# Optimization experiments

Hardware: AMD Instinct MI355X
Metric: run time of the kernel (lower is better)

Reference implementation:

```python
import jax, jax.numpy as jnp
import numpy as np

D_MODEL = 2048
D_STATE = 16
D_CONV = 4
EXPAND = 2
D_INNER = EXPAND * D_MODEL  # 4096
DT_RANK = 128               # ceil(2048/16)
BATCH = 2
SEQ = 1024


def setup_inputs() -> dict:
    key = jax.random.key(0)
    ks = jax.random.split(key, 10)
    n = lambda k, shape, scale: jax.random.normal(k, shape, dtype=jnp.float32) * scale
    # A_log = log(arange(1..N)) broadcast over channels, exactly as in the torch init
    A_log = jnp.log(jnp.tile(jnp.arange(1, D_STATE + 1, dtype=jnp.float32)[None, :], (D_INNER, 1)))
    return {
        "hidden_states": n(ks[0], (BATCH, SEQ, D_MODEL), 1.0),
        "W_in": n(ks[1], (2 * D_INNER, D_MODEL), 0.02),
        "conv_w": n(ks[2], (D_INNER, D_CONV), 0.2),
        "conv_b": n(ks[3], (D_INNER,), 0.02),
        "W_x": n(ks[4], (DT_RANK + 2 * D_STATE, D_INNER), 0.02),
        "W_dt": n(ks[5], (D_INNER, DT_RANK), 0.05),
        "b_dt": n(ks[6], (D_INNER,), 0.5) - 4.0,  # softplus(b_dt) ~ small dt, like inv-softplus init
        "A_log": A_log,
        "D_skip": jnp.ones((D_INNER,), jnp.float32),
        "W_out": n(ks[7], (D_MODEL, D_INNER), 0.02),
    }


def _mamba_forward(hidden_states, W_in, conv_w, conv_b, W_x, W_dt, b_dt, A_log, D_skip, W_out):
    B, L, _ = hidden_states.shape
    # in_proj then split into x (SSM path) and z (gate)
    xz = hidden_states @ W_in.T                      # (B, L, 2*Di)
    x, z = jnp.split(xz, 2, axis=-1)                 # (B, L, Di) each
    # causal depthwise conv1d (kernel D_CONV, left pad D_CONV-1) + SiLU
    xp = jnp.pad(x, ((0, 0), (D_CONV - 1, 0), (0, 0)))
    xc = conv_b
    for k in range(D_CONV):
        xc = xc + conv_w[:, k] * xp[:, k:k + L, :]
    x = jax.nn.silu(xc)                              # (B, L, Di)
    # input-dependent dt, B, C
    x_dbl = x @ W_x.T                                # (B, L, dt_rank + 2N)
    dt_low, B_in, C_in = jnp.split(x_dbl, [DT_RANK, DT_RANK + D_STATE], axis=-1)
    dt = dt_low @ W_dt.T                             # (B, L, Di); bias added inside scan (delta_bias)
    delta = jax.nn.softplus(dt + b_dt)               # (B, L, Di)
    A = -jnp.exp(A_log)                              # (Di, N)

    def step(h, inp):
        delta_t, u_t, B_t, C_t = inp                 # (B,Di),(B,Di),(B,N),(B,N)
        dA = jnp.exp(delta_t[..., None] * A)         # (B, Di, N)
        h = dA * h + (delta_t * u_t)[..., None] * B_t[:, None, :]
        y_t = jnp.einsum('bdn,bn->bd', h, C_t)
        return h, y_t

    h0 = jnp.zeros((B, D_INNER, D_STATE), x.dtype)
    xs = (jnp.swapaxes(delta, 0, 1), jnp.swapaxes(x, 0, 1),
          jnp.swapaxes(B_in, 0, 1), jnp.swapaxes(C_in, 0, 1))
    _, ys = jax.lax.scan(step, h0, xs)               # ys: (L, B, Di)
    y = jnp.swapaxes(ys, 0, 1)                       # (B, L, Di)
    y = y + D_skip * x                               # skip connection
    y = y * jax.nn.silu(z)                           # output gating
    return y @ W_out.T                               # (B, L, D_MODEL)


def reference(hidden_states, W_in, conv_w, conv_b, W_x, W_dt, b_dt, A_log, D_skip, W_out):
    return _mamba_forward(hidden_states, W_in, conv_w, conv_b, W_x, W_dt, b_dt, A_log, D_skip, W_out)
```

## Files before the change

### kernel.cpp

```cpp
#include <hip/hip_runtime.h>
#include <hip/hip_bf16.h>


#define BATCH 2
#define SEQ 1024
#define DMODEL 2048
#define DINNER 4096
#define DSTATE 16
#define DTRANK 128
#define ROWS (BATCH * SEQ)
#define XDBL_N (DTRANK + 2 * DSTATE)
#define NCHUNK 32
#define LOG2_NCHUNK 5
#define CLEN (SEQ / NCHUNK)
#define WXPAD 192
#define SPLITK 16

typedef unsigned short ushort_t;
typedef __attribute__((ext_vector_type(8))) short short8;
typedef __attribute__((ext_vector_type(4))) float f32x4;

__device__ __forceinline__ ushort_t bf16_rne(float f) {
  unsigned u = __float_as_uint(f);
  return (ushort_t)((u + 0x7FFFu + ((u >> 16) & 1u)) >> 16);
}

__global__ __launch_bounds__(256) void cast_bf16(
    const float* __restrict__ x, ushort_t* __restrict__ o, int n4) {
  int i = blockIdx.x * 256 + threadIdx.x;
  if (i >= n4) return;
  float4 v = ((const float4*)x)[i];
  ushort4 h;
  h.x = bf16_rne(v.x); h.y = bf16_rne(v.y);
  h.z = bf16_rne(v.z); h.w = bf16_rne(v.w);
  ((ushort4*)o)[i] = h;
}

__global__ __launch_bounds__(256) void cast_wx(
    const float* __restrict__ wx, ushort_t* __restrict__ o) {
  int i = blockIdx.x * 256 + threadIdx.x;
  if (i >= WXPAD * (DINNER / 4)) return;
  int row = i >> 10;
  ushort4 h = {0, 0, 0, 0};
  if (row < XDBL_N) {
    float4 v = ((const float4*)wx)[i];
    h.x = bf16_rne(v.x); h.y = bf16_rne(v.y);
    h.z = bf16_rne(v.z); h.w = bf16_rne(v.w);
  }
  ((ushort4*)o)[i] = h;
}

template <int TM, int TN, int EPI, bool SK, bool SWZ>
__global__ __launch_bounds__(256, 2) void gemm_bf16(
    const ushort_t* __restrict__ X, int lda,
    const ushort_t* __restrict__ W, int ldb,
    const float* __restrict__ bias,
    float* __restrict__ C, int ldc, int kslice, size_t sstride) {
  constexpr int MI = TM / 32;
  constexpr int NI = TN / 32;
  constexpr int G = (TM + TN) / 32;
  __shared__ __attribute__((aligned(16))) ushort_t lds[(TM + TN) * 64];

  const int tid = threadIdx.x;
  const int lane = tid & 63;
  const int w = tid >> 6;
  const int wm = w & 1, wn = w >> 1;
  int bx = blockIdx.x, by = blockIdx.y;
  if (SWZ) {
    const int bid = by * 16 + bx;
    const int cpx = (16 * gridDim.y) >> 3;
    const int sz = (bid & 7) * cpx + (bid >> 3);
    bx = sz & 15;
    by = sz >> 4;
  }
  const int m0 = bx * TM;
  const int n0 = by * TN;
  const int kbase = SK ? blockIdx.z * kslice : 0;

  const int lrow = lane >> 3;
  const int csw = (lane & 7) ^ lrow;
  const int quad = lane >> 4;
  const int l15 = lane & 15;
  const int x0 = quad ^ (lane & 7);
  const int baseA = (wm * (TM / 2) + l15) * 64;
  const int baseB = (TM + wn * (TN / 2) + l15) * 64;

  f32x4 acc[MI][NI] = {};

  for (int kt = 0; kt < kslice; kt += 64) {
#pragma unroll
    for (int j = 0; j < G; j++) {
      const int r0 = (w * G + j) * 8;
      const int row = r0 + lrow;
      const ushort_t* src = (r0 < TM)
          ? X + (size_t)(m0 + row) * lda + kbase + kt + csw * 8
          : W + (size_t)(n0 + row - TM) * ldb + kbase + kt + csw * 8;
      __builtin_amdgcn_global_load_lds(
          (const __attribute__((address_space(1))) unsigned int*)src,
          (__attribute__((address_space(3))) unsigned int*)&lds[r0 * 64],
          16, 0, 0);
    }
    __syncthreads();

#pragma unroll
    for (int ks = 0; ks < 2; ks++) {
      const int xo = (x0 ^ (ks * 4)) * 8;
      short8 a[MI], b[NI];
#pragma unroll
      for (int mi = 0; mi < MI; mi++)
        a[mi] = *(const short8*)&lds[baseA + mi * 1024 + xo];
#pragma unroll
      for (int ni = 0; ni < NI; ni++)
        b[ni] = *(const short8*)&lds[baseB + ni * 1024 + xo];
#pragma unroll
      for (int mi = 0; mi < MI; mi++)
#pragma unroll
        for (int ni = 0; ni < NI; ni++)
          acc[mi][ni] = __builtin_amdgcn_mfma_f32_16x16x32_bf16(
              a[mi], b[ni], acc[mi][ni], 0, 0, 0);
    }
    __syncthreads();
  }

  float* Cs = SK ? (C + (size_t)blockIdx.z * sstride) : C;
#pragma unroll
  for (int mi = 0; mi < MI; mi++)
#pragma unroll
    for (int ni = 0; ni < NI; ni++) {
      int row = m0 + wm * (TM / 2) + mi * 16 + quad * 4;
      int col = n0 + wn * (TN / 2) + ni * 16 + l15;
#pragma unroll
      for (int r = 0; r < 4; r++) {
        float v = acc[mi][ni][r];
        if (EPI == 1) {
          v += bias[col];
          v = (v > 20.f) ? v : log1pf(__expf(v));
        }
        Cs[(size_t)(row + r) * ldc + col] = v;
      }
    }
}

__device__ __forceinline__ void bar() {
  asm volatile("" ::: "memory");
  __builtin_amdgcn_s_barrier();
  asm volatile("" ::: "memory");
}
#define VMWAIT(n) asm volatile("s_waitcnt vmcnt(" #n ")" ::: "memory")
#define LGKM0 asm volatile("s_waitcnt lgkmcnt(0)" ::: "memory")
#define LGKM8 asm volatile("s_waitcnt lgkmcnt(8)" ::: "memory")
#define SCHED0 __builtin_amdgcn_sched_barrier(0)

#define CLUSTER(AF, BF, MH, NH)                                           \
  do {                                                                    \
    __builtin_amdgcn_s_setprio(1);                                        \
    _Pragma("unroll")                                                     \
    for (int mi = 0; mi < 4; mi++)                                        \
      _Pragma("unroll")                                                   \
      for (int ni = 0; ni < 2; ni++)                                      \
        _Pragma("unroll")                                                 \
        for (int ks = 0; ks < 2; ks++)                                    \
          acc[(MH) * 4 + mi][(NH) * 2 + ni] =                             \
              __builtin_amdgcn_mfma_f32_16x16x32_bf16(                    \
                  AF[mi][ks], BF[ni][ks],                                 \
                  acc[(MH) * 4 + mi][(NH) * 2 + ni], 0, 0, 0);            \
    __builtin_amdgcn_s_setprio(0);                                        \
  } while (0)

#define RD_A(buf, half)                                                   \
  _Pragma("unroll")                                                       \
  for (int mi = 0; mi < 4; mi++)                                          \
    _Pragma("unroll")                                                     \
    for (int ks = 0; ks < 2; ks++) a[mi][ks] = rdA(buf, half, mi, ks)

#define RD_B(dst, buf, nh)                                                \
  _Pragma("unroll")                                                       \
  for (int ni = 0; ni < 2; ni++)                                          \
    _Pragma("unroll")                                                     \
    for (int ks = 0; ks < 2; ks++) dst[ni][ks] = rdB(buf, nh, ni, ks)

__global__ __launch_bounds__(512, 2) void gemm256(
    const ushort_t* __restrict__ X, int lda,
    const ushort_t* __restrict__ W, int ldb,
    float* __restrict__ C, int ldc, int K) {
  __shared__ __attribute__((aligned(16))) ushort_t lds[65536];
  const int tid = threadIdx.x;
  const int lane = tid & 63;
  const int w = tid >> 6;
  const int wm = w >> 2, wn = w & 3;
  const int bid = blockIdx.y * 8 + blockIdx.x;
  const int swz = (bid & 7) * 32 + (bid >> 3);
  const int m0 = (swz & 7) * 256;
  const int n0 = (swz >> 3) * 256;
  const int lrow = lane >> 3;
  const int csw = (lane & 7) ^ lrow;
  const int quad = lane >> 4;
  const int l15 = lane & 15;
  const int sx = lane & 7;

  f32x4 acc[8][4] = {};
  short8 a[4][2], b0[2][2], b1[2][2];

  const ushort_t* Asrc = X + (size_t)(m0 + w * 8 + lrow) * lda + csw * 8;
  const ushort_t* Bsrc = W + (size_t)(n0 + w * 8 + lrow) * ldb + csw * 8;

  auto stA = [&](int buf, int g, int kt) {
    __builtin_amdgcn_global_load_lds(
        (const __attribute__((address_space(1))) unsigned int*)
            (Asrc + (size_t)g * 64 * lda + kt),
        (__attribute__((address_space(3))) unsigned int*)
            &lds[buf * 16384 + (g * 64 + w * 8) * 64],
        16, 0, 0);
  };
  auto stB = [&](int buf, int g, int kt) {
    __builtin_amdgcn_global_load_lds(
        (const __attribute__((address_space(1))) unsigned int*)
            (Bsrc + (size_t)g * 64 * ldb + kt),
        (__attribute__((address_space(3))) unsigned int*)
            &lds[32768 + buf * 16384 + (g * 64 + w * 8) * 64],
        16, 0, 0);
  };
  auto rdA = [&](int buf, int half, int mi, int ks) {
    int row = wm * 128 + half * 64 + mi * 16 + l15;
    int ch = (ks * 4 + quad) ^ sx;
    return *(const short8*)&lds[buf * 16384 + row * 64 + ch * 8];
  };
  auto rdB = [&](int buf, int nh, int ni, int ks) {
    int row = nh * 128 + wn * 32 + ni * 16 + l15;
    int ch = (ks * 4 + quad) ^ sx;
    return *(const short8*)&lds[32768 + buf * 16384 + row * 64 + ch * 8];
  };

#pragma unroll
  for (int g = 0; g < 4; g++) stA(0, g, 0);
#pragma unroll
  for (int g = 0; g < 4; g++) stB(0, g, 0);
  stA(1, 0, 64); stA(1, 2, 64);
  stB(1, 0, 64); stB(1, 1, 64);
  stB(1, 2, 64); stB(1, 3, 64);
  VMWAIT(0);
  bar();

  const int NI = K / 128;
  for (int i = 0; i < NI - 1; ++i) {
    const int k1 = (2 * i + 1) * 64;
    const int ks0 = (2 * i + 2) * 64;
    const int ks1 = (2 * i + 3) * 64;
    RD_A(0, 0); RD_B(b0, 0, 0);
    stA(1, 1, k1); stA(1, 3, k1);
    LGKM8;
    bar(); LGKM0; SCHED0;
    CLUSTER(a, b0, 0, 0);
    bar();
    RD_B(b1, 0, 1);
    stA(0, 0, ks0); stA(0, 2, ks0);
    bar(); LGKM0; SCHED0;
    CLUSTER(a, b1, 0, 1);
    bar();
    RD_A(0, 1);
    stB(0, 0, ks0); stB(0, 1, ks0);
    bar(); LGKM0; SCHED0;
    CLUSTER(a, b1, 1, 1);
    bar();
    stB(0, 2, ks0); stB(0, 3, ks0);
    bar(); SCHED0;
    CLUSTER(a, b0, 1, 0);
    VMWAIT(6);
    bar();
    RD_A(1, 0); RD_B(b0, 1, 0);
    stA(0, 1, ks0); stA(0, 3, ks0);
    LGKM8;
    bar(); LGKM0; SCHED0;
    CLUSTER(a, b0, 0, 0);
    bar();
    RD_B(b1, 1, 1);
    stA(1, 0, ks1); stA(1, 2, ks1);
    bar(); LGKM0; SCHED0;
    CLUSTER(a, b1, 0, 1);
    bar();
    RD_A(1, 1);
    stB(1, 0, ks1); stB(1, 1, ks1);
    bar(); LGKM0; SCHED0;
    CLUSTER(a, b1, 1, 1);
    bar();
    stB(1, 2, ks1); stB(1, 3, ks1);
    bar(); SCHED0;
    CLUSTER(a, b0, 1, 0);
    VMWAIT(6);
    bar();
  }
  {
    const int k1 = (K / 64 - 1) * 64;
    RD_A(0, 0); RD_B(b0, 0, 0);
    stA(1, 1, k1); stA(1, 3, k1);
    LGKM8;
    bar(); LGKM0; SCHED0;
    CLUSTER(a, b0, 0, 0);
    bar();
    RD_B(b1, 0, 1);
    bar(); LGKM0; SCHED0;
    CLUSTER(a, b1, 0, 1);
    bar();
    RD_A(0, 1);
    bar(); LGKM0; SCHED0;
    CLUSTER(a, b1, 1, 1);
    bar();
    SCHED0;
    CLUSTER(a, b0, 1, 0);
    VMWAIT(0);
    bar();
    RD_A(1, 0); RD_B(b0, 1, 0);
    LGKM8;
    bar(); LGKM0; SCHED0;
    CLUSTER(a, b0, 0, 0);
    bar();
    RD_B(b1, 1, 1);
    bar(); LGKM0; SCHED0;
    CLUSTER(a, b1, 0, 1);
    bar();
    RD_A(1, 1);
    bar(); LGKM0; SCHED0;
    CLUSTER(a, b1, 1, 1);
    CLUSTER(a, b0, 1, 0);
  }

#pragma unroll
  for (int mj = 0; mj < 8; mj++)
#pragma unroll
    for (int nj = 0; nj < 4; nj++) {
      int row = m0 + wm * 128 + mj * 16 + quad * 4;
      int col = n0 + (nj >> 1) * 128 + wn * 32 + (nj & 1) * 16 + l15;
#pragma unroll
      for (int r = 0; r < 4; r++)
        C[(size_t)(row + r) * ldc + col] = acc[mj][nj][r];
    }
}

__global__ __launch_bounds__(192) void reduce_sk(
    const float* __restrict__ partials, float* __restrict__ xdbl,
    ushort_t* __restrict__ dtb) {
  int m = blockIdx.x;
  int c = threadIdx.x;
  if (c >= XDBL_N) return;
  float s = 0.f;
#pragma unroll
  for (int z = 0; z < SPLITK; z++)
    s += partials[(size_t)z * ROWS * WXPAD + (size_t)m * WXPAD + c];
  xdbl[(size_t)m * XDBL_N + c] = s;
  if (c < DTRANK) dtb[(size_t)m * DTRANK + c] = bf16_rne(s);
}

__global__ __launch_bounds__(256) void conv_silu(
    const float* __restrict__ xz, const float* __restrict__ cw,
    const float* __restrict__ cb, float* __restrict__ xs,
    ushort_t* __restrict__ xsb) {
  int idx = blockIdx.x * 256 + threadIdx.x;
  if (idx >= ROWS * DINNER / 4) return;
  int d4 = idx & (DINNER / 4 - 1);
  int bt = idx >> 10;
  int t = bt & (SEQ - 1);
  int d = d4 * 4;
  float4 c4 = *(const float4*)&cb[d];
  float wv[4][4];
  *(float4*)wv[0] = *(const float4*)&cw[(d + 0) * 4];
  *(float4*)wv[1] = *(const float4*)&cw[(d + 1) * 4];
  *(float4*)wv[2] = *(const float4*)&cw[(d + 2) * 4];
  *(float4*)wv[3] = *(const float4*)&cw[(d + 3) * 4];
  float a0 = c4.x, a1 = c4.y, a2 = c4.z, a3 = c4.w;
#pragma unroll
  for (int k = 0; k < 4; k++) {
    int tt = t - 3 + k;
    if (tt >= 0) {
      float4 v = *(const float4*)&xz[(size_t)(bt - 3 + k) * (2 * DINNER) + d];
      a0 += wv[0][k] * v.x;
      a1 += wv[1][k] * v.y;
      a2 += wv[2][k] * v.z;
      a3 += wv[3][k] * v.w;
    }
  }
  float4 s;
  s.x = a0 / (1.f + __expf(-a0));
  s.y = a1 / (1.f + __expf(-a1));
  s.z = a2 / (1.f + __expf(-a2));
  s.w = a3 / (1.f + __expf(-a3));
  *(float4*)&xs[(size_t)bt * DINNER + d] = s;
  ushort4 h;
  h.x = bf16_rne(s.x); h.y = bf16_rne(s.y);
  h.z = bf16_rne(s.z); h.w = bf16_rne(s.w);
  *(ushort4*)&xsb[(size_t)bt * DINNER + d] = h;
}

__global__ __launch_bounds__(256) void scan_pass1(
    const float* __restrict__ delta, const float* __restrict__ xs,
    const float* __restrict__ xdbl, const float* __restrict__ A_log,
    float* __restrict__ hpart, float* __restrict__ sumd) {
  int g = blockIdx.x * 256 + threadIdx.x;
  int d = g & (DINNER - 1);
  int rest = g >> 12;
  int c = rest & (NCHUNK - 1);
  int b = rest >> LOG2_NCHUNK;

  float Adn[16];
#pragma unroll
  for (int q = 0; q < 4; q++) {
    float4 a = *(const float4*)&A_log[d * 16 + q * 4];
    Adn[q * 4 + 0] = -__expf(a.x); Adn[q * 4 + 1] = -__expf(a.y);
    Adn[q * 4 + 2] = -__expf(a.z); Adn[q * 4 + 3] = -__expf(a.w);
  }

  float h[16] = {};
  float sd = 0.f;
  const size_t t0 = (size_t)b * SEQ + c * CLEN;
  const float* dp = delta + t0 * DINNER + d;
  const float* up = xs + t0 * DINNER + d;
  const float* xb = xdbl + t0 * XDBL_N + DTRANK;

  for (int i = 0; i < CLEN; i++) {
    float dt = dp[(size_t)i * DINNER];
    float u = up[(size_t)i * DINNER];
    sd += dt;
    float du = dt * u;
    float Bv[16];
#pragma unroll
    for (int q = 0; q < 4; q++)
      *(float4*)&Bv[q * 4] = *(const float4*)&xb[i * XDBL_N + q * 4];
#pragma unroll
    for (int n = 0; n < 16; n++)
      h[n] = __expf(dt * Adn[n]) * h[n] + du * Bv[n];
  }

  float* hp = hpart + ((size_t)(c * BATCH + b) * DINNER + d) * 16;
#pragma unroll
  for (int q = 0; q < 4; q++) *(float4*)&hp[q * 4] = *(const float4*)&h[q * 4];
  sumd[(size_t)(c * BATCH + b) * DINNER + d] = sd;
}

__global__ __launch_bounds__(256) void scan_pass2(
    float* __restrict__ hph, const float* __restrict__ sumd,
    const float* __restrict__ A_log) {
  int g = blockIdx.x * 256 + threadIdx.x;
  int n = g & 15;
  int d = (g >> 4) & (DINNER - 1);
  int b = g >> 16;

  float Adn = -__expf(A_log[d * 16 + n]);
  float h = 0.f;
  for (int c = 0; c < NCHUNK; c++) {
    size_t base = (size_t)(c * BATCH + b) * DINNER + d;
    float part = hph[base * 16 + n];
    hph[base * 16 + n] = h;
    h = __expf(Adn * sumd[base]) * h + part;
  }
}

__global__ __launch_bounds__(256) void scan_pass3(
    const float* __restrict__ xz, const float* __restrict__ xs,
    const float* __restrict__ xdbl, const float* __restrict__ A_log,
    const float* __restrict__ D_skip, const float* __restrict__ h0,
    const float* __restrict__ delta, ushort_t* __restrict__ gated) {
  int g = blockIdx.x * 256 + threadIdx.x;
  int d = g & (DINNER - 1);
  int rest = g >> 12;
  int c = rest & (NCHUNK - 1);
  int b = rest >> LOG2_NCHUNK;

  float Adn[16];
#pragma unroll
  for (int q = 0; q < 4; q++) {
    float4 a = *(const float4*)&A_log[d * 16 + q * 4];
    Adn[q * 4 + 0] = -__expf(a.x); Adn[q * 4 + 1] = -__expf(a.y);
    Adn[q * 4 + 2] = -__expf(a.z); Adn[q * 4 + 3] = -__expf(a.w);
  }
  float Dd = D_skip[d];

  float h[16];
  const float* hp = h0 + ((size_t)(c * BATCH + b) * DINNER + d) * 16;
#pragma unroll
  for (int q = 0; q < 4; q++) *(float4*)&h[q * 4] = *(const float4*)&hp[q * 4];

  const size_t t0 = (size_t)b * SEQ + c * CLEN;
  const float* dl = delta + t0 * DINNER + d;
  const float* up = xs + t0 * DINNER + d;
  const float* zb = xz + t0 * (2 * DINNER) + DINNER + d;
  const float* xb = xdbl + t0 * XDBL_N + DTRANK;
  ushort_t* gp = gated + t0 * DINNER + d;

  for (int i = 0; i < CLEN; i++) {
    float dt = dl[(size_t)i * DINNER];
    float u = up[(size_t)i * DINNER];
    float du = dt * u;
    float Bv[16], Cv[16];
#pragma unroll
    for (int q = 0; q < 4; q++) {
      *(float4*)&Bv[q * 4] = *(const float4*)&xb[i * XDBL_N + q * 4];
      *(float4*)&Cv[q * 4] = *(const float4*)&xb[i * XDBL_N + DSTATE + q * 4];
    }
    float y = 0.f;
#pragma unroll
    for (int n = 0; n < 16; n++) {
      h[n] = __expf(dt * Adn[n]) * h[n] + du * Bv[n];
      y += h[n] * Cv[n];
    }
    float z = zb[(size_t)i * (2 * DINNER)];
    float sz = z / (1.f + __expf(-z));
    gp[(size_t)i * DINNER] = bf16_rne((y + Dd * u) * sz);
  }
}

extern "C" void kernel_launch(void* const* d_in, const int* in_sizes, int n_in,
                              void* d_out, int out_size, void* d_ws, size_t ws_size,
                              hipStream_t stream) {
  const float* hidden = (const float*)d_in[0];
  const float* W_in   = (const float*)d_in[1];
  const float* conv_w = (const float*)d_in[2];
  const float* conv_b = (const float*)d_in[3];
  const float* W_x    = (const float*)d_in[4];
  const float* W_dt   = (const float*)d_in[5];
  const float* b_dt   = (const float*)d_in[6];
  const float* A_log  = (const float*)d_in[7];
  const float* D_skip = (const float*)d_in[8];
  const float* W_out  = (const float*)d_in[9];
  float* out = (float*)d_out;

  float* ws    = (float*)d_ws;
  float* xz    = ws;
  float* xs    = xz + (size_t)ROWS * 2 * DINNER;
  float* xdbl  = xs + (size_t)ROWS * DINNER;
  float* delta = xdbl + (size_t)ROWS * XDBL_N;
  float* sumd  = delta + (size_t)ROWS * DINNER;
  float* hph   = sumd + (size_t)BATCH * DINNER * NCHUNK;
  ushort_t* Hb   = (ushort_t*)(hph + (size_t)BATCH * DINNER * NCHUNK * DSTATE);
  ushort_t* Wb1  = Hb + (size_t)ROWS * DMODEL;
  ushort_t* Wxb  = Wb1 + (size_t)2 * DINNER * DMODEL;
  ushort_t* Wdtb = Wxb + (size_t)WXPAD * DINNER;
  ushort_t* xsb  = Wdtb + (size_t)DINNER * DTRANK;
  ushort_t* dtb  = xsb + (size_t)ROWS * DINNER;
  float* partials = (float*)Wb1;
  ushort_t* Woutb = Wb1;
  ushort_t* gatedb = Wb1 + (size_t)DMODEL * DINNER;

  dim3 blk(256);

  cast_bf16<<<(ROWS * DMODEL / 4 + 255) / 256, blk, 0, stream>>>(
      hidden, Hb, ROWS * DMODEL / 4);
  cast_bf16<<<(2 * DINNER * DMODEL / 4 + 255) / 256, blk, 0, stream>>>(
      W_in, Wb1, 2 * DINNER * DMODEL / 4);

  gemm256<<<dim3(8, 32), dim3(512), 0, stream>>>(
      Hb, DMODEL, Wb1, DMODEL, xz, 2 * DINNER, DMODEL);

  conv_silu<<<(ROWS * DINNER / 4 + 255) / 256, blk, 0, stream>>>(
      xz, conv_w, conv_b, xs, xsb);

  cast_wx<<<(WXPAD * DINNER / 4 + 255) / 256, blk, 0, stream>>>(W_x, Wxb);
  cast_bf16<<<(DINNER * DTRANK / 4 + 255) / 256, blk, 0, stream>>>(
      W_dt, Wdtb, DINNER * DTRANK / 4);

  gemm_bf16<128, 64, 0, true, false><<<dim3(16, 3, SPLITK), blk, 0, stream>>>(
      xsb, DINNER, Wxb, DINNER, nullptr, partials, WXPAD, DINNER / SPLITK,
      (size_t)ROWS * WXPAD);
  reduce_sk<<<ROWS, dim3(WXPAD), 0, stream>>>(partials, xdbl, dtb);

  gemm_bf16<128, 128, 1, false, true><<<dim3(16, 32), blk, 0, stream>>>(
      dtb, DTRANK, Wdtb, DTRANK, b_dt, delta, DINNER, DTRANK, 0);

  scan_pass1<<<(BATCH * DINNER * NCHUNK) / 256, blk, 0, stream>>>(
      delta, xs, xdbl, A_log, hph, sumd);
  scan_pass2<<<(BATCH * DINNER * DSTATE) / 256, blk, 0, stream>>>(
      hph, sumd, A_log);
  scan_pass3<<<(BATCH * DINNER * NCHUNK) / 256, blk, 0, stream>>>(
      xz, xs, xdbl, A_log, D_skip, hph, delta, gatedb);

  cast_bf16<<<(DMODEL * DINNER / 4 + 255) / 256, blk, 0, stream>>>(
      W_out, Woutb, DMODEL * DINNER / 4);

  gemm_bf16<128, 64, 0, false, true><<<dim3(16, 32), blk, 0, stream>>>(
      gatedb, DINNER, Woutb, DINNER, nullptr, out, DMODEL, DINNER, 0);
}
```

Baseline: 451.0 us.

## Batch weight casts into one launch and split-K the output projection

Merges the four fp32-to-bf16 cast kernels (hidden states, W_in, W_dt, W_out) into a single cast_batch launch issued up front, with W_out given its own workspace slot so it no longer aliases Wb1. The output projection now uses 128x128 tiles with 2-way split-K writing partials into the xz buffer, followed by a reduce2 kernel that sums them. This cuts launch count and raises block-level parallelism for the final GEMM, at the cost of an extra fp32 partial write and read plus one more reduction kernel.

Result: faster. 438.8 us (-2.7%).

```diff
diff --git a/kernel.cpp b/kernel.cpp
--- a/kernel.cpp
+++ b/kernel.cpp
@@ -25,15 +25,27 @@
   return (ushort_t)((u + 0x7FFFu + ((u >> 16) & 1u)) >> 16);
 }
 
-__global__ __launch_bounds__(256) void cast_bf16(
-    const float* __restrict__ x, ushort_t* __restrict__ o, int n4) {
-  int i = blockIdx.x * 256 + threadIdx.x;
-  if (i >= n4) return;
-  float4 v = ((const float4*)x)[i];
+__device__ __forceinline__ void cast4(const float* s, ushort_t* d, int i) {
+  float4 v = ((const float4*)s)[i];
   ushort4 h;
   h.x = bf16_rne(v.x); h.y = bf16_rne(v.y);
   h.z = bf16_rne(v.z); h.w = bf16_rne(v.w);
-  ((ushort4*)o)[i] = h;
+  ((ushort4*)d)[i] = h;
+}
+
+__global__ __launch_bounds__(256) void cast_batch(
+    const float* __restrict__ s0, ushort_t* __restrict__ d0, int n0,
+    const float* __restrict__ s1, ushort_t* __restrict__ d1, int n1,
+    const float* __restrict__ s2, ushort_t* __restrict__ d2, int n2,
+    const float* __restrict__ s3, ushort_t* __restrict__ d3, int n3) {
+  int i = blockIdx.x * 256 + threadIdx.x;
+  if (i < n0) { cast4(s0, d0, i); return; }
+  i -= n0;
+  if (i < n1) { cast4(s1, d1, i); return; }
+  i -= n1;
+  if (i < n2) { cast4(s2, d2, i); return; }
+  i -= n2;
+  if (i < n3) cast4(s3, d3, i);
 }
 
 __global__ __launch_bounds__(256) void cast_wx(
@@ -48,6 +60,17 @@
     h.z = bf16_rne(v.z); h.w = bf16_rne(v.w);
   }
   ((ushort4*)o)[i] = h;
+}
+
+__global__ __launch_bounds__(256) void reduce2(
+    const float* __restrict__ p, float* __restrict__ out, int n4) {
+  int i = blockIdx.x * 256 + threadIdx.x;
+  if (i >= n4) return;
+  float4 a = ((const float4*)p)[i];
+  float4 b = ((const float4*)(p + (size_t)ROWS * DMODEL))[i];
+  float4 r;
+  r.x = a.x + b.x; r.y = a.y + b.y; r.z = a.z + b.z; r.w = a.w + b.w;
+  ((float4*)out)[i] = r;
 }
 
 template <int TM, int TN, int EPI, bool SK, bool SWZ>
@@ -535,26 +558,28 @@
   ushort_t* Wdtb = Wxb + (size_t)WXPAD * DINNER;
   ushort_t* xsb  = Wdtb + (size_t)DINNER * DTRANK;
   ushort_t* dtb  = xsb + (size_t)ROWS * DINNER;
+  ushort_t* Woutb = dtb + (size_t)ROWS * DTRANK;
   float* partials = (float*)Wb1;
-  ushort_t* Woutb = Wb1;
   ushort_t* gatedb = Wb1 + (size_t)DMODEL * DINNER;
+  float* partials4 = xz;
 
   dim3 blk(256);
 
-  cast_bf16<<<(ROWS * DMODEL / 4 + 255) / 256, blk, 0, stream>>>(
-      hidden, Hb, ROWS * DMODEL / 4);
-  cast_bf16<<<(2 * DINNER * DMODEL / 4 + 255) / 256, blk, 0, stream>>>(
-      W_in, Wb1, 2 * DINNER * DMODEL / 4);
+  {
+    int n0 = ROWS * DMODEL / 4;
+    int n1 = 2 * DINNER * DMODEL / 4;
+    int n2 = DINNER * DTRANK / 4;
+    int n3 = DMODEL * DINNER / 4;
+    cast_batch<<<(n0 + n1 + n2 + n3 + 255) / 256, blk, 0, stream>>>(
+        hidden, Hb, n0, W_in, Wb1, n1, W_dt, Wdtb, n2, W_out, Woutb, n3);
+  }
+  cast_wx<<<(WXPAD * DINNER / 4 + 255) / 256, blk, 0, stream>>>(W_x, Wxb);
 
   gemm256<<<dim3(8, 32), dim3(512), 0, stream>>>(
       Hb, DMODEL, Wb1, DMODEL, xz, 2 * DINNER, DMODEL);
 
   conv_silu<<<(ROWS * DINNER / 4 + 255) / 256, blk, 0, stream>>>(
       xz, conv_w, conv_b, xs, xsb);
-
-  cast_wx<<<(WXPAD * DINNER / 4 + 255) / 256, blk, 0, stream>>>(W_x, Wxb);
-  cast_bf16<<<(DINNER * DTRANK / 4 + 255) / 256, blk, 0, stream>>>(
-      W_dt, Wdtb, DINNER * DTRANK / 4);
 
   gemm_bf16<128, 64, 0, true, false><<<dim3(16, 3, SPLITK), blk, 0, stream>>>(
       xsb, DINNER, Wxb, DINNER, nullptr, partials, WXPAD, DINNER / SPLITK,
@@ -571,9 +596,9 @@
   scan_pass3<<<(BATCH * DINNER * NCHUNK) / 256, blk, 0, stream>>>(
       xz, xs, xdbl, A_log, D_skip, hph, delta, gatedb);
 
-  cast_bf16<<<(DMODEL * DINNER / 4 + 255) / 256, blk, 0, stream>>>(
-      W_out, Woutb, DMODEL * DINNER / 4);
-
-  gemm_bf16<128, 64, 0, false, true><<<dim3(16, 32), blk, 0, stream>>>(
-      gatedb, DINNER, Woutb, DINNER, nullptr, out, DMODEL, DINNER, 0);
-}
+  gemm_bf16<128, 128, 0, true, true><<<dim3(16, 16, 2), blk, 0, stream>>>(
+      gatedb, DINNER, Woutb, DINNER, nullptr, partials4, DMODEL, DINNER / 2,
+      (size_t)ROWS * DMODEL);
+  reduce2<<<(ROWS * DMODEL / 4 + 255) / 256, blk, 0, stream>>>(
+      partials4, out, ROWS * DMODEL / 4);
+}
```
